# Performance work log

Hardware: AMD Instinct MI355X
Metric: run time of the kernel (lower is better)

Reference implementation:

```python
import jax, jax.numpy as jnp
import numpy as np

N_WIRES = 4
N_LAYERS = 3
BATCH = 65536
BN_EPS = 1e-5


def setup_inputs() -> dict:
    key = jax.random.key(0)
    k = jax.random.split(key, 4)
    return {
        "x": jax.random.normal(k[0], (BATCH, 1, 28, 28), dtype=jnp.float32),
        "params": jax.random.normal(k[1], (N_LAYERS, N_WIRES, 3), dtype=jnp.float32),
        "W": jax.random.normal(k[2], (4, N_WIRES), dtype=jnp.float32) * 0.5,
        "b": jax.random.normal(k[3], (4,), dtype=jnp.float32) * 0.1,
        "bn_weight": jnp.ones((4,), dtype=jnp.float32),
        "bn_bias": jnp.zeros((4,), dtype=jnp.float32),
    }


def _fused_rzrx(params):
    """Precompute M[l,w] = RX(params[l,w,1]) @ RZ(params[l,w,0]); shape (L,W,2,2) complex.
    (params[...,2] is unused by the original circuit.)"""
    t0 = params[..., 0]
    t1 = params[..., 1]
    ez = jnp.exp(-0.5j * t0)          # RZ diag entries: (ez, conj(ez))
    ezc = jnp.exp(0.5j * t0)
    cx = jnp.cos(0.5 * t1) + 0j
    sx = -1j * jnp.sin(0.5 * t1)
    row0 = jnp.stack([cx * ez, sx * ezc], axis=-1)
    row1 = jnp.stack([sx * ez, cx * ezc], axis=-1)
    return jnp.stack([row0, row1], axis=-2).astype(jnp.complex64)


def _ry(t):
    c = jnp.cos(0.5 * t) + 0j
    s = jnp.sin(0.5 * t) + 0j
    return jnp.stack([jnp.stack([c, -s]), jnp.stack([s, c])]).astype(jnp.complex64)


def _sim_one(xv, M):
    """Statevector simulation of the 4-wire variational circuit for one sample.
    xv: (4,) encoding angles; M: (L,W,2,2) fused RX@RZ gates. Returns (4,) PauliZ expvals."""
    state = jnp.zeros((2,) * N_WIRES, dtype=jnp.complex64).at[0, 0, 0, 0].set(1.0)
    rys = [_ry(xv[w]) for w in range(N_WIRES)]
    for i in range(N_LAYERS):
        for w in range(N_WIRES):
            U = M[i, w] @ rys[w]  # RY then RZ then RX, fused into one 2x2
            state = jnp.moveaxis(jnp.tensordot(U, state, axes=([1], [w])), 0, w)
            if w < N_WIRES - 1:
                # CNOT(control=w, target=w+1): flip target amps where control=1
                s = jnp.moveaxis(state, (w, w + 1), (0, 1))
                s = s.at[1].set(s[1, ::-1])
                state = jnp.moveaxis(s, (0, 1), (w, w + 1))
    probs = jnp.real(state * jnp.conj(state))  # (2,2,2,2)
    zs = []
    for w in range(N_WIRES):
        other = tuple(a for a in range(N_WIRES) if a != w)
        m = probs.sum(axis=other)  # marginal over wire w
        zs.append(m[0] - m[1])
    return jnp.stack(zs)


def reference(x, params, W, b, bn_weight, bn_bias):
    bsz = x.shape[0]
    flat = x.reshape(bsz, -1)
    # chunk into 4 equal groups and mean each -> (B, 4) encoding angles
    enc = flat.reshape(bsz, N_WIRES, -1).mean(axis=-1)
    M = _fused_rzrx(params)
    z = jax.vmap(_sim_one, in_axes=(0, None))(enc, M).astype(jnp.float32)  # (B, 4)
    out = z @ W.T + b  # Linear(4, 4)
    # BatchNorm1d (training mode, biased variance)
    mu = out.mean(axis=0)
    var = ((out - mu) ** 2).mean(axis=0)
    return (out - mu) * jax.lax.rsqrt(var + BN_EPS) * bn_weight + bn_bias
```

## Files before the change

kernel.cpp:

```cpp
#include <hip/hip_runtime.h>

#define BN_EPS 1e-5f

__global__ __launch_bounds__(256) void encode_kernel(const float* __restrict__ x,
                                                     float* __restrict__ enc) {
    int wave = (int)((blockIdx.x * blockDim.x + threadIdx.x) >> 6);
    int lane = threadIdx.x & 63;
    const float4* xs = (const float4*)(x + (size_t)wave * 784);

    float4 v0 = xs[lane];
    float4 v1 = xs[64 + lane];
    float4 v2 = xs[128 + lane];
    float4 v3 = (lane < 4) ? xs[192 + lane] : make_float4(0.f, 0.f, 0.f, 0.f);

    float t0 = (v0.x + v0.y) + (v0.z + v0.w);
    float t1 = (v1.x + v1.y) + (v1.z + v1.w);
    float t2 = (v2.x + v2.y) + (v2.z + v2.w);
    float t3 = (v3.x + v3.y) + (v3.z + v3.w);

    float s0 = (lane < 49) ? t0 : 0.f;
    float s1 = ((lane >= 49) ? t0 : 0.f) + ((lane < 34) ? t1 : 0.f);
    float s2 = ((lane >= 34) ? t1 : 0.f) + ((lane < 19) ? t2 : 0.f);
    float s3 = ((lane >= 19) ? t2 : 0.f) + t3;

#pragma unroll
    for (int off = 32; off > 0; off >>= 1) {
        s0 += __shfl_down(s0, off);
        s1 += __shfl_down(s1, off);
        s2 += __shfl_down(s2, off);
        s3 += __shfl_down(s3, off);
    }
    if (lane == 0) {
        const float inv = 1.0f / 196.0f;
        ((float4*)enc)[wave] = make_float4(s0 * inv, s1 * inv, s2 * inv, s3 * inv);
    }
}

__global__ __launch_bounds__(256) void sim_kernel(const float* __restrict__ enc,
                                                  const float* __restrict__ params,
                                                  const float* __restrict__ Wm,
                                                  const float* __restrict__ bvec,
                                                  float* __restrict__ out_ws,
                                                  float* __restrict__ sums) {
    __shared__ float G[96];
    __shared__ float WB[20];
    if (threadIdx.x < 12) {
        int t = threadIdx.x;
        float t0 = params[t * 3 + 0];
        float t1 = params[t * 3 + 1];
        float s0, c0, s1, c1;
        __sincosf(0.5f * t0, &s0, &c0);
        __sincosf(0.5f * t1, &s1, &c1);
        float* m = G + t * 8;
        m[0] = c1 * c0;   m[1] = -c1 * s0;
        m[2] = s1 * s0;   m[3] = -s1 * c0;
        m[4] = -s1 * s0;  m[5] = -s1 * c0;
        m[6] = c1 * c0;   m[7] = c1 * s0;
    } else if (threadIdx.x < 32) {
        int k = threadIdx.x - 12;
        if (k < 16) WB[k] = Wm[k];
        else WB[k] = bvec[k - 16];
    }
    __syncthreads();

    int t = blockIdx.x * blockDim.x + threadIdx.x;
    float4 e = ((const float4*)enc)[t];
    float ang[4] = {e.x, e.y, e.z, e.w};
    float cw[4], sw[4];
#pragma unroll
    for (int w = 0; w < 4; w++) __sincosf(0.5f * ang[w], &sw[w], &cw[w]);

    float sr[16], si[16];
#pragma unroll
    for (int i = 0; i < 16; i++) { sr[i] = 0.f; si[i] = 0.f; }
    sr[0] = 1.0f;

#pragma unroll
    for (int l = 0; l < 3; l++) {
#pragma unroll
        for (int w = 0; w < 4; w++) {
            const float* m = G + (l * 4 + w) * 8;
            float c = cw[w], s = sw[w];
            float u00r = m[0] * c + m[2] * s;
            float u00i = m[1] * c + m[3] * s;
            float u01r = -m[0] * s + m[2] * c;
            float u01i = -m[1] * s + m[3] * c;
            float u10r = m[4] * c + m[6] * s;
            float u10i = m[5] * c + m[7] * s;
            float u11r = -m[4] * s + m[6] * c;
            float u11i = -m[5] * s + m[7] * c;
            const int stride = 8 >> w;
#pragma unroll
            for (int i = 0; i < 16; i++) {
                if (i & stride) continue;
                int j = i | stride;
                float a0r = sr[i], a0i = si[i];
                float a1r = sr[j], a1i = si[j];
                sr[i] = u00r * a0r - u00i * a0i + u01r * a1r - u01i * a1i;
                si[i] = u00r * a0i + u00i * a0r + u01r * a1i + u01i * a1r;
                sr[j] = u10r * a0r - u10i * a0i + u11r * a1r - u11i * a1i;
                si[j] = u10r * a0i + u10i * a0r + u11r * a1i + u11i * a1r;
            }
            if (w < 3) {
                const int ts = 8 >> (w + 1);
#pragma unroll
                for (int i = 0; i < 16; i++) {
                    if (!(i & stride)) continue;
                    if (i & ts) continue;
                    int j = i | ts;
                    float tr = sr[i]; sr[i] = sr[j]; sr[j] = tr;
                    float ti = si[i]; si[i] = si[j]; si[j] = ti;
                }
            }
        }
    }

    float p[16];
#pragma unroll
    for (int i = 0; i < 16; i++) p[i] = sr[i] * sr[i] + si[i] * si[i];
    float z[4];
#pragma unroll
    for (int w = 0; w < 4; w++) {
        const int stride = 8 >> w;
        float acc = 0.f;
#pragma unroll
        for (int i = 0; i < 16; i++) acc += (i & stride) ? -p[i] : p[i];
        z[w] = acc;
    }

    float o[4];
#pragma unroll
    for (int j = 0; j < 4; j++) {
        o[j] = WB[16 + j] + WB[j * 4 + 0] * z[0] + WB[j * 4 + 1] * z[1] +
               WB[j * 4 + 2] * z[2] + WB[j * 4 + 3] * z[3];
    }
    ((float4*)out_ws)[t] = make_float4(o[0], o[1], o[2], o[3]);

    float vals[8];
#pragma unroll
    for (int j = 0; j < 4; j++) { vals[j] = o[j]; vals[4 + j] = o[j] * o[j]; }
#pragma unroll
    for (int k = 0; k < 8; k++) {
#pragma unroll
        for (int off = 32; off > 0; off >>= 1) vals[k] += __shfl_down(vals[k], off);
    }
    __shared__ float part[4][8];
    int lane = threadIdx.x & 63;
    int wv = threadIdx.x >> 6;
    if (lane == 0) {
#pragma unroll
        for (int k = 0; k < 8; k++) part[wv][k] = vals[k];
    }
    __syncthreads();
    if (threadIdx.x == 0) {
#pragma unroll
        for (int k = 0; k < 8; k++) {
            float tsum = part[0][k] + part[1][k] + part[2][k] + part[3][k];
            atomicAdd(&sums[k], tsum);
        }
    }
}

__global__ __launch_bounds__(256) void norm_kernel(const float* __restrict__ out_ws,
                                                   const float* __restrict__ sums,
                                                   const float* __restrict__ bn_w,
                                                   const float* __restrict__ bn_b,
                                                   float* __restrict__ dout,
                                                   float inv_batch) {
    __shared__ float sc[4], sh[4];
    if (threadIdx.x < 4) {
        int j = threadIdx.x;
        float mu = sums[j] * inv_batch;
        float ex2 = sums[4 + j] * inv_batch;
        float var = ex2 - mu * mu;
        float s = bn_w[j] * rsqrtf(var + BN_EPS);
        sc[j] = s;
        sh[j] = bn_b[j] - mu * s;
    }
    __syncthreads();
    int t = blockIdx.x * blockDim.x + threadIdx.x;
    float4 o = ((const float4*)out_ws)[t];
    ((float4*)dout)[t] = make_float4(o.x * sc[0] + sh[0], o.y * sc[1] + sh[1],
                                     o.z * sc[2] + sh[2], o.w * sc[3] + sh[3]);
}

extern "C" void kernel_launch(void* const* d_in, const int* in_sizes, int n_in,
                              void* d_out, int out_size, void* d_ws, size_t ws_size,
                              hipStream_t stream) {
    const float* x      = (const float*)d_in[0];
    const float* params = (const float*)d_in[1];
    const float* Wm     = (const float*)d_in[2];
    const float* bvec   = (const float*)d_in[3];
    const float* bn_w   = (const float*)d_in[4];
    const float* bn_b   = (const float*)d_in[5];
    float* dout = (float*)d_out;

    const int B = in_sizes[0] / 784;

    float* ws   = (float*)d_ws;
    float* sums = ws;
    float* enc  = ws + 64;
    float* outw = ws + 64 + 4 * (size_t)B;

    hipMemsetAsync(sums, 0, 8 * sizeof(float), stream);
    encode_kernel<<<B / 4, 256, 0, stream>>>(x, enc);
    sim_kernel<<<B / 256, 256, 0, stream>>>(enc, params, Wm, bvec, outw, sums);
    norm_kernel<<<B / 256, 256, 0, stream>>>(outw, sums, bn_w, bn_b, dout, 1.0f / (float)B);
}
```

Before: 319.1 us.

## Fuse encode and simulation kernels; replace atomics with per-block partials

Merges the pixel-mean encoding and the statevector simulation into one kernel of 1024 blocks. Each block's four waves reduce 64 images into shared memory, then one wave simulates the circuit. This drops the global encoding buffer round trip and the separate launch. The memset and atomicAdd accumulation are replaced by per-block partial sums, which every norm block reduces redundantly. The trade-off is fewer independent waves streaming the input, so memory parallelism may drop. The grid size is also hardcoded to match the batch of 65536.

After: 298.0 us. -6.6%, faster.

```diff
diff --git a/kernel.cpp b/kernel.cpp
--- a/kernel.cpp
+++ b/kernel.cpp
@@ -1,187 +1,202 @@
 #include <hip/hip_runtime.h>
 
 #define BN_EPS 1e-5f
-
-__global__ __launch_bounds__(256) void encode_kernel(const float* __restrict__ x,
-                                                     float* __restrict__ enc) {
-    int wave = (int)((blockIdx.x * blockDim.x + threadIdx.x) >> 6);
-    int lane = threadIdx.x & 63;
-    const float4* xs = (const float4*)(x + (size_t)wave * 784);
-
-    float4 v0 = xs[lane];
-    float4 v1 = xs[64 + lane];
-    float4 v2 = xs[128 + lane];
-    float4 v3 = (lane < 4) ? xs[192 + lane] : make_float4(0.f, 0.f, 0.f, 0.f);
-
-    float t0 = (v0.x + v0.y) + (v0.z + v0.w);
-    float t1 = (v1.x + v1.y) + (v1.z + v1.w);
-    float t2 = (v2.x + v2.y) + (v2.z + v2.w);
-    float t3 = (v3.x + v3.y) + (v3.z + v3.w);
-
-    float s0 = (lane < 49) ? t0 : 0.f;
-    float s1 = ((lane >= 49) ? t0 : 0.f) + ((lane < 34) ? t1 : 0.f);
-    float s2 = ((lane >= 34) ? t1 : 0.f) + ((lane < 19) ? t2 : 0.f);
-    float s3 = ((lane >= 19) ? t2 : 0.f) + t3;
-
-#pragma unroll
-    for (int off = 32; off > 0; off >>= 1) {
-        s0 += __shfl_down(s0, off);
-        s1 += __shfl_down(s1, off);
-        s2 += __shfl_down(s2, off);
-        s3 += __shfl_down(s3, off);
-    }
-    if (lane == 0) {
-        const float inv = 1.0f / 196.0f;
-        ((float4*)enc)[wave] = make_float4(s0 * inv, s1 * inv, s2 * inv, s3 * inv);
-    }
-}
-
-__global__ __launch_bounds__(256) void sim_kernel(const float* __restrict__ enc,
-                                                  const float* __restrict__ params,
-                                                  const float* __restrict__ Wm,
-                                                  const float* __restrict__ bvec,
-                                                  float* __restrict__ out_ws,
-                                                  float* __restrict__ sums) {
+#define NBLK 1024
+
+__global__ __launch_bounds__(256) void encode_sim_kernel(
+    const float* __restrict__ x,
+    const float* __restrict__ params,
+    const float* __restrict__ Wm,
+    const float* __restrict__ bvec,
+    float* __restrict__ out_ws,
+    float* __restrict__ partials) {
     __shared__ float G[96];
-    __shared__ float WB[20];
-    if (threadIdx.x < 12) {
-        int t = threadIdx.x;
-        float t0 = params[t * 3 + 0];
-        float t1 = params[t * 3 + 1];
+    __shared__ float encl[64][5];
+
+    const int tid  = threadIdx.x;
+    const int lane = tid & 63;
+    const int wv   = tid >> 6;
+    const int b    = blockIdx.x;
+    const int base = b * 64;
+
+    if (tid < 12) {
+        float t0 = params[tid * 3 + 0];
+        float t1 = params[tid * 3 + 1];
         float s0, c0, s1, c1;
         __sincosf(0.5f * t0, &s0, &c0);
         __sincosf(0.5f * t1, &s1, &c1);
-        float* m = G + t * 8;
+        float* m = G + tid * 8;
         m[0] = c1 * c0;   m[1] = -c1 * s0;
         m[2] = s1 * s0;   m[3] = -s1 * c0;
         m[4] = -s1 * s0;  m[5] = -s1 * c0;
         m[6] = c1 * c0;   m[7] = c1 * s0;
-    } else if (threadIdx.x < 32) {
-        int k = threadIdx.x - 12;
-        if (k < 16) WB[k] = Wm[k];
-        else WB[k] = bvec[k - 16];
-    }
-    __syncthreads();
-
-    int t = blockIdx.x * blockDim.x + threadIdx.x;
-    float4 e = ((const float4*)enc)[t];
-    float ang[4] = {e.x, e.y, e.z, e.w};
-    float cw[4], sw[4];
-#pragma unroll
-    for (int w = 0; w < 4; w++) __sincosf(0.5f * ang[w], &sw[w], &cw[w]);
-
-    float sr[16], si[16];
-#pragma unroll
-    for (int i = 0; i < 16; i++) { sr[i] = 0.f; si[i] = 0.f; }
-    sr[0] = 1.0f;
-
-#pragma unroll
-    for (int l = 0; l < 3; l++) {
-#pragma unroll
-        for (int w = 0; w < 4; w++) {
-            const float* m = G + (l * 4 + w) * 8;
-            float c = cw[w], s = sw[w];
-            float u00r = m[0] * c + m[2] * s;
-            float u00i = m[1] * c + m[3] * s;
-            float u01r = -m[0] * s + m[2] * c;
-            float u01i = -m[1] * s + m[3] * c;
-            float u10r = m[4] * c + m[6] * s;
-            float u10i = m[5] * c + m[7] * s;
-            float u11r = -m[4] * s + m[6] * c;
-            float u11i = -m[5] * s + m[7] * c;
-            const int stride = 8 >> w;
-#pragma unroll
-            for (int i = 0; i < 16; i++) {
-                if (i & stride) continue;
-                int j = i | stride;
-                float a0r = sr[i], a0i = si[i];
-                float a1r = sr[j], a1i = si[j];
-                sr[i] = u00r * a0r - u00i * a0i + u01r * a1r - u01i * a1i;
-                si[i] = u00r * a0i + u00i * a0r + u01r * a1i + u01i * a1r;
-                sr[j] = u10r * a0r - u10i * a0i + u11r * a1r - u11i * a1i;
-                si[j] = u10r * a0i + u10i * a0r + u11r * a1i + u11i * a1r;
-            }
-            if (w < 3) {
-                const int ts = 8 >> (w + 1);
+    }
+
+#pragma unroll 2
+    for (int i = 0; i < 16; i++) {
+        int sl = wv * 16 + i;
+        const float4* xs = (const float4*)(x + (size_t)(base + sl) * 784);
+        float4 v0 = xs[lane];
+        float4 v1 = xs[64 + lane];
+        float4 v2 = xs[128 + lane];
+        float4 v3 = (lane < 4) ? xs[192 + lane] : make_float4(0.f, 0.f, 0.f, 0.f);
+
+        float t0 = (v0.x + v0.y) + (v0.z + v0.w);
+        float t1 = (v1.x + v1.y) + (v1.z + v1.w);
+        float t2 = (v2.x + v2.y) + (v2.z + v2.w);
+        float t3 = (v3.x + v3.y) + (v3.z + v3.w);
+
+        float s0 = (lane < 49) ? t0 : 0.f;
+        float s1 = ((lane >= 49) ? t0 : 0.f) + ((lane < 34) ? t1 : 0.f);
+        float s2 = ((lane >= 34) ? t1 : 0.f) + ((lane < 19) ? t2 : 0.f);
+        float s3 = ((lane >= 19) ? t2 : 0.f) + t3;
+
+#pragma unroll
+        for (int off = 32; off > 0; off >>= 1) {
+            s0 += __shfl_down(s0, off);
+            s1 += __shfl_down(s1, off);
+            s2 += __shfl_down(s2, off);
+            s3 += __shfl_down(s3, off);
+        }
+        if (lane == 0) {
+            const float inv = 1.0f / 196.0f;
+            encl[sl][0] = s0 * inv;
+            encl[sl][1] = s1 * inv;
+            encl[sl][2] = s2 * inv;
+            encl[sl][3] = s3 * inv;
+        }
+    }
+    __syncthreads();
+
+    if (wv == 0) {
+        float ang[4] = {encl[lane][0], encl[lane][1], encl[lane][2], encl[lane][3]};
+        float cw[4], sw[4];
+#pragma unroll
+        for (int w = 0; w < 4; w++) __sincosf(0.5f * ang[w], &sw[w], &cw[w]);
+
+        float sr[16], si[16];
+#pragma unroll
+        for (int i = 0; i < 16; i++) { sr[i] = 0.f; si[i] = 0.f; }
+        sr[0] = 1.0f;
+
+#pragma unroll
+        for (int l = 0; l < 3; l++) {
+#pragma unroll
+            for (int w = 0; w < 4; w++) {
+                const float* m = G + (l * 4 + w) * 8;
+                float c = cw[w], s = sw[w];
+                float u00r = m[0] * c + m[2] * s;
+                float u00i = m[1] * c + m[3] * s;
+                float u01r = -m[0] * s + m[2] * c;
+                float u01i = -m[1] * s + m[3] * c;
+                float u10r = m[4] * c + m[6] * s;
+                float u10i = m[5] * c + m[7] * s;
+                float u11r = -m[4] * s + m[6] * c;
+                float u11i = -m[5] * s + m[7] * c;
+                const int stride = 8 >> w;
 #pragma unroll
                 for (int i = 0; i < 16; i++) {
-                    if (!(i & stride)) continue;
-                    if (i & ts) continue;
-                    int j = i | ts;
-                    float tr = sr[i]; sr[i] = sr[j]; sr[j] = tr;
-                    float ti = si[i]; si[i] = si[j]; si[j] = ti;
+                    if (i & stride) continue;
+                    int j = i | stride;
+                    float a0r = sr[i], a0i = si[i];
+                    float a1r = sr[j], a1i = si[j];
+                    sr[i] = u00r * a0r - u00i * a0i + u01r * a1r - u01i * a1i;
+                    si[i] = u00r * a0i + u00i * a0r + u01r * a1i + u01i * a1r;
+                    sr[j] = u10r * a0r - u10i * a0i + u11r * a1r - u11i * a1i;
+                    si[j] = u10r * a0i + u10i * a0r + u11r * a1i + u11i * a1r;
+                }
+                if (w < 3) {
+                    const int ts = 8 >> (w + 1);
+#pragma unroll
+                    for (int i = 0; i < 16; i++) {
+                        if (!(i & stride)) continue;
+                        if (i & ts) continue;
+                        int j = i | ts;
+                        float tr = sr[i]; sr[i] = sr[j]; sr[j] = tr;
+                        float ti = si[i]; si[i] = si[j]; si[j] = ti;
+                    }
                 }
             }
         }
-    }
-
-    float p[16];
-#pragma unroll
-    for (int i = 0; i < 16; i++) p[i] = sr[i] * sr[i] + si[i] * si[i];
-    float z[4];
-#pragma unroll
-    for (int w = 0; w < 4; w++) {
-        const int stride = 8 >> w;
+
+        float p[16];
+#pragma unroll
+        for (int i = 0; i < 16; i++) p[i] = sr[i] * sr[i] + si[i] * si[i];
+        float z[4];
+#pragma unroll
+        for (int w = 0; w < 4; w++) {
+            const int stride = 8 >> w;
+            float acc = 0.f;
+#pragma unroll
+            for (int i = 0; i < 16; i++) acc += (i & stride) ? -p[i] : p[i];
+            z[w] = acc;
+        }
+
+        float o[4];
+#pragma unroll
+        for (int j = 0; j < 4; j++) {
+            o[j] = bvec[j] + Wm[j * 4 + 0] * z[0] + Wm[j * 4 + 1] * z[1] +
+                   Wm[j * 4 + 2] * z[2] + Wm[j * 4 + 3] * z[3];
+        }
+        ((float4*)out_ws)[base + lane] = make_float4(o[0], o[1], o[2], o[3]);
+
+        float vals[8];
+#pragma unroll
+        for (int j = 0; j < 4; j++) { vals[j] = o[j]; vals[4 + j] = o[j] * o[j]; }
+#pragma unroll
+        for (int k = 0; k < 8; k++) {
+#pragma unroll
+            for (int off = 32; off > 0; off >>= 1) vals[k] += __shfl_down(vals[k], off);
+        }
+        if (lane == 0) {
+#pragma unroll
+            for (int k = 0; k < 8; k++) partials[b * 8 + k] = vals[k];
+        }
+    }
+}
+
+__global__ __launch_bounds__(256) void norm_kernel(
+    const float* __restrict__ out_ws,
+    const float* __restrict__ partials,
+    const float* __restrict__ bn_w,
+    const float* __restrict__ bn_b,
+    float* __restrict__ dout,
+    float inv_batch) {
+    __shared__ float red[32][8];
+    __shared__ float scsh[8];
+    const int tid = threadIdx.x;
+
+    {
+        int f = tid & 7, row = tid >> 3;
         float acc = 0.f;
-#pragma unroll
-        for (int i = 0; i < 16; i++) acc += (i & stride) ? -p[i] : p[i];
-        z[w] = acc;
-    }
-
-    float o[4];
-#pragma unroll
-    for (int j = 0; j < 4; j++) {
-        o[j] = WB[16 + j] + WB[j * 4 + 0] * z[0] + WB[j * 4 + 1] * z[1] +
-               WB[j * 4 + 2] * z[2] + WB[j * 4 + 3] * z[3];
-    }
-    ((float4*)out_ws)[t] = make_float4(o[0], o[1], o[2], o[3]);
-
-    float vals[8];
-#pragma unroll
-    for (int j = 0; j < 4; j++) { vals[j] = o[j]; vals[4 + j] = o[j] * o[j]; }
-#pragma unroll
-    for (int k = 0; k < 8; k++) {
-#pragma unroll
-        for (int off = 32; off > 0; off >>= 1) vals[k] += __shfl_down(vals[k], off);
-    }
-    __shared__ float part[4][8];
-    int lane = threadIdx.x & 63;
-    int wv = threadIdx.x >> 6;
-    if (lane == 0) {
-#pragma unroll
-        for (int k = 0; k < 8; k++) part[wv][k] = vals[k];
-    }
-    __syncthreads();
-    if (threadIdx.x == 0) {
-#pragma unroll
-        for (int k = 0; k < 8; k++) {
-            float tsum = part[0][k] + part[1][k] + part[2][k] + part[3][k];
-            atomicAdd(&sums[k], tsum);
-        }
-    }
-}
-
-__global__ __launch_bounds__(256) void norm_kernel(const float* __restrict__ out_ws,
-                                                   const float* __restrict__ sums,
-                                                   const float* __restrict__ bn_w,
-                                                   const float* __restrict__ bn_b,
-                                                   float* __restrict__ dout,
-                                                   float inv_batch) {
-    __shared__ float sc[4], sh[4];
-    if (threadIdx.x < 4) {
-        int j = threadIdx.x;
-        float mu = sums[j] * inv_batch;
-        float ex2 = sums[4 + j] * inv_batch;
+#pragma unroll 4
+        for (int i = 0; i < NBLK / 32; i++) acc += partials[(row + 32 * i) * 8 + f];
+        red[row][f] = acc;
+    }
+    __syncthreads();
+    if (tid < 8) {
+        float t = 0.f;
+#pragma unroll
+        for (int r = 0; r < 32; r++) t += red[r][tid];
+        red[0][tid] = t;
+    }
+    __syncthreads();
+    if (tid < 4) {
+        float mu = red[0][tid] * inv_batch;
+        float ex2 = red[0][tid + 4] * inv_batch;
         float var = ex2 - mu * mu;
-        float s = bn_w[j] * rsqrtf(var + BN_EPS);
-        sc[j] = s;
-        sh[j] = bn_b[j] - mu * s;
-    }
-    __syncthreads();
-    int t = blockIdx.x * blockDim.x + threadIdx.x;
+        float s = bn_w[tid] * rsqrtf(var + BN_EPS);
+        scsh[tid] = s;
+        scsh[4 + tid] = bn_b[tid] - mu * s;
+    }
+    __syncthreads();
+
+    int t = blockIdx.x * blockDim.x + tid;
     float4 o = ((const float4*)out_ws)[t];
-    ((float4*)dout)[t] = make_float4(o.x * sc[0] + sh[0], o.y * sc[1] + sh[1],
-                                     o.z * sc[2] + sh[2], o.w * sc[3] + sh[3]);
+    ((float4*)dout)[t] = make_float4(o.x * scsh[0] + scsh[4],
+                                     o.y * scsh[1] + scsh[5],
+                                     o.z * scsh[2] + scsh[6],
+                                     o.w * scsh[3] + scsh[7]);
 }
 
 extern "C" void kernel_launch(void* const* d_in, const int* in_sizes, int n_in,
@@ -197,13 +212,11 @@
 
     const int B = in_sizes[0] / 784;
 
-    float* ws   = (float*)d_ws;
-    float* sums = ws;
-    float* enc  = ws + 64;
-    float* outw = ws + 64 + 4 * (size_t)B;
-
-    hipMemsetAsync(sums, 0, 8 * sizeof(float), stream);
-    encode_kernel<<<B / 4, 256, 0, stream>>>(x, enc);
-    sim_kernel<<<B / 256, 256, 0, stream>>>(enc, params, Wm, bvec, outw, sums);
-    norm_kernel<<<B / 256, 256, 0, stream>>>(outw, sums, bn_w, bn_b, dout, 1.0f / (float)B);
+    float* ws       = (float*)d_ws;
+    float* partials = ws;
+    float* outw     = ws + NBLK * 8;
+
+    encode_sim_kernel<<<NBLK, 256, 0, stream>>>(x, params, Wm, bvec, outw, partials);
+    norm_kernel<<<B / 256, 256, 0, stream>>>(outw, partials, bn_w, bn_b, dout,
+                                             1.0f / (float)B);
 }
```
